# Performance work log

Hardware: AMD Instinct MI355X
Metric: run time of the kernel (lower is better)

## Reference

```python
import jax, jax.numpy as jnp
import numpy as np

N_TEXT = 80000
N_NON = 20000
N = N_TEXT + N_NON
E = 200000
EMB = 256
HID = 256
R = 500
V = 17
MDIM = 64
K = 4
NUM_ROUNDS = 2
NUM_REV_ROUNDS = 2


def setup_inputs():
    key = jax.random.key(0)
    ks = jax.random.split(key, 32)
    f = jnp.float32
    s = 0.05
    inp = {}
    inp["h_id_tensor"] = jax.random.randint(ks[0], (E,), 0, N)
    inp["r_id_tensor"] = jax.random.randint(ks[1], (E,), 0, R)
    inp["t_id_tensor"] = jax.random.randint(ks[2], (E,), 0, N)
    inp["q_emb"] = jax.random.normal(ks[3], (1, EMB), f)
    inp["entity_embs"] = jax.random.normal(ks[4], (N_TEXT, EMB), f)
    inp["num_non_text_entities"] = N_NON
    inp["relation_embs"] = jax.random.normal(ks[5], (R, EMB), f)
    inp["topic_entity_one_hot"] = (jax.random.uniform(ks[6], (N, 2)) < 0.01).astype(f)
    inp["node_motif_token_ids"] = jax.random.randint(ks[7], (N, K), 0, V)
    inp["node_motif_token_wts"] = jax.random.uniform(ks[8], (N, K), f)
    inp["triple_motif_token_ids"] = jax.random.randint(ks[9], (E, K), 0, V)
    inp["triple_motif_token_wts"] = jax.random.uniform(ks[10], (E, K), f)
    inp["non_text_emb"] = jax.random.normal(ks[11], (EMB,), f) * s
    me = jax.random.normal(ks[12], (V, MDIM), f) * s
    inp["motif_emb"] = me.at[0].set(0.0)  # padding_idx=0
    inp["gnn_self_w"] = jax.random.normal(ks[13], (MDIM, MDIM), f) * s
    inp["gnn_self_b"] = jnp.zeros((MDIM,), f)
    inp["gnn_msg_w"] = jax.random.normal(ks[14], (MDIM, MDIM), f) * s
    inp["gnn_msg_b"] = jnp.zeros((MDIM,), f)
    pos_dim = 2 + 2 * (NUM_ROUNDS + NUM_REV_ROUNDS)  # 10
    inp["nh_w"] = jax.random.normal(ks[15], (2 * EMB + 2 * MDIM, HID), f) * s
    inp["nh_b"] = jnp.zeros((HID,), f)
    inp["pos_w"] = jax.random.normal(ks[16], (2 * pos_dim, HID), f) * s
    inp["pos_b"] = jnp.zeros((HID,), f)
    inp["st_w"] = jax.random.normal(ks[17], (EMB + MDIM, HID), f) * s
    inp["st_b"] = jnp.zeros((HID,), f)
    inp["gate_w"] = jax.random.normal(ks[18], (EMB, 3), f) * s
    inp["gate_b"] = jnp.zeros((3,), f)
    inp["pred_w1"] = jax.random.normal(ks[19], (EMB + HID, HID), f) * s
    inp["pred_b1"] = jnp.zeros((HID,), f)
    inp["pred_w2"] = jax.random.normal(ks[20], (HID, 1), f) * s
    inp["pred_b2"] = jnp.zeros((1,), f)
    return inp


def _forward(h_id, r_id, t_id, q_emb, entity_embs, num_non_text, relation_embs,
             topic_oh, node_ids, node_wts, trip_ids, trip_wts,
             non_text_emb, motif_emb, gsw, gsb, gmw, gmb,
             nh_w, nh_b, pos_w, pos_b, st_w, st_b, gate_w, gate_b,
             pw1, pb1, pw2, pb2):
    n = entity_embs.shape[0] + num_non_text
    h_e = jnp.concatenate(
        [entity_embs,
         jnp.broadcast_to(non_text_emb[None, :], (num_non_text, entity_embs.shape[1]))],
        axis=0)  # [N, EMB]
    ones = jnp.ones((h_id.shape[0],), h_e.dtype)
    inv_fwd = 1.0 / jnp.clip(jax.ops.segment_sum(ones, t_id, num_segments=n), 1.0)[:, None]
    inv_rev = 1.0 / jnp.clip(jax.ops.segment_sum(ones, h_id, num_segments=n), 1.0)[:, None]

    def mean_agg(x, src, dst, inv):
        # PyG mean aggregation: mean of source features over incoming edges, 0 if none
        return jax.ops.segment_sum(x[src], dst, num_segments=n) * inv

    dde_list = []
    h = topic_oh
    for _ in range(NUM_ROUNDS):
        h = mean_agg(h, h_id, t_id, inv_fwd)
        dde_list.append(h)
    h = topic_oh
    for _ in range(NUM_REV_ROUNDS):
        h = mean_agg(h, t_id, h_id, inv_rev)
        dde_list.append(h)

    # ---- motif co-occurrence adjacency (vectorized form of the K x K loop) ----
    contrib = trip_wts[:, :, None] * trip_wts[:, None, :]                 # [E,K,K]
    valid = (trip_ids[:, :, None] > 0) & (trip_ids[:, None, :] > 0) & (contrib > 0)
    contrib = jnp.where(valid, contrib, 0.0)
    idx = (trip_ids[:, :, None] * V + trip_ids[:, None, :]).reshape(-1)
    adj = jnp.zeros((V * V,), contrib.dtype).at[idx].add(contrib.reshape(-1)).reshape(V, V)
    adj = 0.5 * (adj + adj.T) + jnp.eye(V, dtype=adj.dtype)
    adj = adj.at[0, :].set(0.0).at[:, 0].set(0.0).at[0, 0].set(1.0)
    adj = adj / jnp.clip(adj.sum(axis=1, keepdims=True), 1e-8)

    # ---- semantic GNN over the motif table ----
    ht = motif_emb
    for _ in range(1):  # semantic_gnn_num_layers = 1, dropout 0 (eval)
        msg = adj @ ht
        ht = ht + jax.nn.relu(ht @ gsw + gsb + msg @ gmw + gmb)

    node_motif_emb = (ht[node_ids] * node_wts[:, :, None]).sum(axis=1)    # [N,MDIM]
    triple_motif_emb = (ht[trip_ids] * trip_wts[:, :, None]).sum(axis=1)  # [E,MDIM]

    h_r = relation_embs[r_id]                                             # [E,EMB]
    h_nbr = jax.nn.relu(
        jnp.concatenate([h_e[h_id], h_e[t_id], node_motif_emb[h_id], node_motif_emb[t_id]],
                        axis=1) @ nh_w + nh_b)
    pos_feat = jnp.concatenate([topic_oh] + dde_list, axis=1)             # [N,10]
    h_pos = jax.nn.relu(
        jnp.concatenate([pos_feat[h_id], pos_feat[t_id]], axis=1) @ pos_w + pos_b)
    h_str = jax.nn.relu(jnp.concatenate([h_r, triple_motif_emb], axis=1) @ st_w + st_b)

    gate = jax.nn.softmax((q_emb @ gate_w + gate_b)[0])                   # [3]
    h_fused = gate[0] * h_nbr + gate[1] * h_pos + gate[2] * h_str
    pred_in = jnp.concatenate(
        [jnp.broadcast_to(q_emb, (h_r.shape[0], q_emb.shape[1])), h_fused], axis=1)
    return jax.nn.relu(pred_in @ pw1 + pb1) @ pw2 + pb2                   # [E,1]


def reference(h_id_tensor, r_id_tensor, t_id_tensor, q_emb, entity_embs,
              num_non_text_entities, relation_embs, topic_entity_one_hot,
              node_motif_token_ids, node_motif_token_wts,
              triple_motif_token_ids, triple_motif_token_wts,
              non_text_emb, motif_emb, gnn_self_w, gnn_self_b, gnn_msg_w, gnn_msg_b,
              nh_w, nh_b, pos_w, pos_b, st_w, st_b, gate_w, gate_b,
              pred_w1, pred_b1, pred_w2, pred_b2):
    return _forward(h_id_tensor, r_id_tensor, t_id_tensor, q_emb, entity_embs,
                    num_non_text_entities, relation_embs, topic_entity_one_hot,
                    node_motif_token_ids, node_motif_token_wts,
                    triple_motif_token_ids, triple_motif_token_wts,
                    non_text_emb, motif_emb, gnn_self_w, gnn_self_b, gnn_msg_w, gnn_msg_b,
                    nh_w, nh_b, pos_w, pos_b, st_w, st_b, gate_w, gate_b,
                    pred_w1, pred_b1, pred_w2, pred_b2)
```

## Files before the change

kernel.cpp:

```cpp
#include <hip/hip_runtime.h>
#include <hip/hip_bf16.h>

#define N_TEXT 80000
#define NTOT   100000
#define NE     200000
#define EMB    256
#define HID    256
#define VMOT   17
#define MDIM   64
#define KTOK   4

typedef unsigned short u16;
typedef unsigned int   u32;
typedef short short8 __attribute__((ext_vector_type(8)));
typedef float f32x4 __attribute__((ext_vector_type(4)));

#define O_INVF 0
#define O_INVR (NTOT)
#define O_POS  (2*NTOT)
#define O_ADJ  (12*NTOT)
#define O_HTB  (12*NTOT + 512)
#define O_GATE (12*NTOT + 1088)
#define O_CVEC (12*NTOT + 1104)
#define O_NME  (12*NTOT + 1360)
#define O_WSW  (O_NME + NTOT*32)
#define ZERO_FLOATS (12*NTOT + 512)
#define Z4 (ZERO_FLOATS/4)

#define GA 20480
#define GB 1024
#define GC 10240
#define GD 8192
#define GTOT (GA+GB+GC+GD)

__device__ __forceinline__ u16 f2b(float f) {
  unsigned u = __float_as_uint(f);
  return (u16)((u + 0x7fffu + ((u >> 16) & 1u)) >> 16);
}
__device__ __forceinline__ float b2f(u16 v) {
  return __uint_as_float(((unsigned)v) << 16);
}
__device__ __forceinline__ short8 pack8f(const float* f) {
  union { u32 u[4]; short8 s; } o;
#pragma unroll
  for (int i = 0; i < 4; i++) {
    __hip_bfloat162 b = __float22bfloat162_rn(float2{f[2*i], f[2*i+1]});
    o.u[i] = *reinterpret_cast<u32*>(&b);
  }
  return o.s;
}

__global__ void k_prep(const float* __restrict__ nh_w, const float* __restrict__ pos_w,
                       const float* __restrict__ st_w, const float* __restrict__ pw1,
                       float* __restrict__ ws) {
  int g = blockIdx.x * blockDim.x + threadIdx.x;
  if (g < Z4) { ((float4*)ws)[g] = make_float4(0.f, 0.f, 0.f, 0.f); return; }
  g -= Z4;
  if (g >= GTOT) return;
  int l, phase;
  if (g < GA) { l = g; phase = 0; }
  else if (g < GA + GB) { l = g - GA; phase = 1; }
  else if (g < GA + GB + GC) { l = g - GA - GB; phase = 2; }
  else { l = g - GA - GB - GC; phase = 3; }
  int c = l >> 10, r = l & 1023;
  int w = r >> 8, nt = (r >> 6) & 3, ln = r & 63;
  int col = w*64 + nt*16 + (ln & 15);
  int k0  = c*32 + ((ln >> 4) << 3);
  float f[8];
#pragma unroll
  for (int j = 0; j < 8; j++) {
    int k = k0 + j;
    float v = 0.f;
    if (phase == 0)      v = nh_w[k*256 + col];
    else if (phase == 1) { if (k < 10) v = pos_w[k*256 + col];
                           else if (k >= 16 && k < 26) v = pos_w[(k-6)*256 + col]; }
    else if (phase == 2) v = st_w[k*256 + col];
    else                 v = pw1[(256 + k)*256 + col];
    f[j] = v;
  }
  ((short8*)((u16*)(ws + O_WSW)))[g] = pack8f(f);
}

__global__ void k_deg_dde1_adj(const int* __restrict__ h_id, const int* __restrict__ t_id,
                               const float* __restrict__ topic,
                               const int* __restrict__ tids, const float* __restrict__ twts,
                               float* __restrict__ ws) {
  __shared__ float sadj[4*304];
  for (int i = threadIdx.x; i < 4*304; i += blockDim.x) sadj[i] = 0.f;
  __syncthreads();
  int wbase = (threadIdx.x >> 6) * 304;
  int e = blockIdx.x * blockDim.x + threadIdx.x;
  if (e < NE) {
    int h = h_id[e], t = t_id[e];
    atomicAdd(&ws[O_INVF + t], 1.0f);
    atomicAdd(&ws[O_INVR + h], 1.0f);
    float hx = topic[2*h], hy = topic[2*h + 1];
    float tx = topic[2*t], ty = topic[2*t + 1];
    if (hx != 0.f) atomicAdd(&ws[O_POS + t*10 + 2], hx);
    if (hy != 0.f) atomicAdd(&ws[O_POS + t*10 + 3], hy);
    if (tx != 0.f) atomicAdd(&ws[O_POS + h*10 + 6], tx);
    if (ty != 0.f) atomicAdd(&ws[O_POS + h*10 + 7], ty);
    int id[KTOK]; float w[KTOK];
#pragma unroll
    for (int k = 0; k < KTOK; k++) { id[k] = tids[e*KTOK + k]; w[k] = twts[e*KTOK + k]; }
#pragma unroll
    for (int i = 0; i < KTOK; i++)
#pragma unroll
      for (int j = 0; j < KTOK; j++) {
        float c = w[i] * w[j];
        if (id[i] > 0 && id[j] > 0 && c > 0.f)
          atomicAdd(&sadj[wbase + id[i]*VMOT + id[j]], c);
      }
  }
  __syncthreads();
  for (int i = threadIdx.x; i < VMOT*VMOT; i += blockDim.x) {
    float v = sadj[i] + sadj[304 + i] + sadj[608 + i] + sadj[912 + i];
    if (v != 0.f) atomicAdd(&ws[O_ADJ + i], v);
  }
}

#define NPN_BLOCKS ((NTOT + 255)/256)
__global__ void k_pnm(const float* __restrict__ topic, const float* __restrict__ mo,
                      const float* __restrict__ gsw, const float* __restrict__ gsb,
                      const float* __restrict__ gmw, const float* __restrict__ gmb,
                      const float* __restrict__ q, const float* __restrict__ gate_w,
                      const float* __restrict__ gate_b, const float* __restrict__ pw1,
                      const float* __restrict__ pb1, float* __restrict__ ws) {
  int t = threadIdx.x;
  if (blockIdx.x < NPN_BLOCKS) {
    int n = blockIdx.x * 256 + t;
    if (n >= NTOT) return;
    float invf = 1.0f / fmaxf(ws[O_INVF + n], 1.0f);
    float invr = 1.0f / fmaxf(ws[O_INVR + n], 1.0f);
    ws[O_INVF + n] = invf;
    ws[O_INVR + n] = invr;
    float* p = &ws[O_POS + n*10];
    p[0] = topic[2*n]; p[1] = topic[2*n + 1];
    p[2] *= invf; p[3] *= invf;
    p[6] *= invr; p[7] *= invr;
  } else if (blockIdx.x == NPN_BLOCKS) {
    __shared__ float A[VMOT*VMOT];
    __shared__ float Bm[VMOT*VMOT];
    __shared__ float inv_row[VMOT];
    __shared__ float smo[VMOT*MDIM];
    __shared__ float sm[VMOT*MDIM];
    for (int i = t; i < VMOT*VMOT; i += 256) A[i] = ws[O_ADJ + i];
    for (int i = t; i < VMOT*MDIM; i += 256) smo[i] = mo[i];
    __syncthreads();
    for (int i = t; i < VMOT*VMOT; i += 256) {
      int r = i / VMOT, c = i % VMOT;
      float v = 0.5f * (A[i] + A[c*VMOT + r]) + (r == c ? 1.f : 0.f);
      if (r == 0 || c == 0) v = (r == 0 && c == 0) ? 1.f : 0.f;
      Bm[i] = v;
    }
    __syncthreads();
    if (t < VMOT) {
      float s = 0.f;
      for (int c = 0; c < VMOT; c++) s += Bm[t*VMOT + c];
      inv_row[t] = 1.f / fmaxf(s, 1e-8f);
    }
    __syncthreads();
    for (int i = t; i < VMOT*MDIM; i += 256) {
      int v = i / MDIM, d = i % MDIM;
      float s = 0.f;
      for (int u = 0; u < VMOT; u++) s += Bm[v*VMOT + u] * smo[u*MDIM + d];
      sm[i] = s * inv_row[v];
    }
    __syncthreads();
    for (int i = t; i < VMOT*MDIM; i += 256) {
      int v = i / MDIM, d = i % MDIM;
      float a = gsb[d] + gmb[d];
      for (int m = 0; m < MDIM; m++)
        a += smo[v*MDIM + m] * gsw[m*MDIM + d] + sm[v*MDIM + m] * gmw[m*MDIM + d];
      ((u16*)(ws + O_HTB))[i] = f2b(smo[i] + fmaxf(a, 0.f));
    }
  } else {
    __shared__ float sq[EMB];
    __shared__ float red[3];
    sq[t] = q[t];
    if (t < 3) red[t] = 0.f;
    __syncthreads();
    float s = pb1[t];
    for (int i = 0; i < EMB; i++) s += sq[i] * pw1[i*HID + t];
    ws[O_CVEC + t] = s;
    atomicAdd(&red[0], sq[t] * gate_w[t*3 + 0]);
    atomicAdd(&red[1], sq[t] * gate_w[t*3 + 1]);
    atomicAdd(&red[2], sq[t] * gate_w[t*3 + 2]);
    __syncthreads();
    if (t == 0) {
      float l0 = red[0] + gate_b[0], l1 = red[1] + gate_b[1], l2 = red[2] + gate_b[2];
      float mx = fmaxf(l0, fmaxf(l1, l2));
      float e0 = expf(l0 - mx), e1 = expf(l1 - mx), e2 = expf(l2 - mx);
      float inv = 1.f / (e0 + e1 + e2);
      ws[O_GATE + 0] = e0 * inv; ws[O_GATE + 1] = e1 * inv; ws[O_GATE + 2] = e2 * inv;
    }
  }
}

__global__ void k_dde2(const int* __restrict__ h_id, const int* __restrict__ t_id,
                       float* __restrict__ ws) {
  int e = blockIdx.x * blockDim.x + threadIdx.x;
  if (e >= NE) return;
  int h = h_id[e], t = t_id[e];
  float a = ws[O_POS + h*10 + 2], b = ws[O_POS + h*10 + 3];
  float c = ws[O_POS + t*10 + 6], d = ws[O_POS + t*10 + 7];
  if (a != 0.f) atomicAdd(&ws[O_POS + t*10 + 4], a);
  if (b != 0.f) atomicAdd(&ws[O_POS + t*10 + 5], b);
  if (c != 0.f) atomicAdd(&ws[O_POS + h*10 + 8], c);
  if (d != 0.f) atomicAdd(&ws[O_POS + h*10 + 9], d);
}

__global__ void k_scale_nme(const int* __restrict__ nids, const float* __restrict__ nwts,
                            float* __restrict__ ws) {
  __shared__ u16 sht[VMOT*MDIM];
  for (int i = threadIdx.x; i < (VMOT*MDIM)/2; i += blockDim.x)
    ((u32*)sht)[i] = ((const u32*)(ws + O_HTB))[i];
  __syncthreads();
  int gid = blockIdx.x * blockDim.x + threadIdx.x;
  if (gid < NTOT) {
    float invf = ws[O_INVF + gid], invr = ws[O_INVR + gid];
    float* p = &ws[O_POS + gid*10];
    p[4] *= invf; p[5] *= invf;
    p[8] *= invr; p[9] *= invr;
  }
  if (gid >= NTOT * 8) return;
  int n = gid >> 3, d0 = (gid & 7) * 8;
  int4   iv = ((const int4*)nids)[n];
  float4 wv = ((const float4*)nwts)[n];
  float f[8];
#pragma unroll
  for (int j = 0; j < 8; j++) {
    f[j] = wv.x * b2f(sht[iv.x*MDIM + d0 + j]) + wv.y * b2f(sht[iv.y*MDIM + d0 + j])
         + wv.z * b2f(sht[iv.z*MDIM + d0 + j]) + wv.w * b2f(sht[iv.w*MDIM + d0 + j]);
  }
  ((short8*)((u16*)(ws + O_NME)))[gid] = pack8f(f);
}

__global__ __launch_bounds__(256, 4) void k_edge_mfma(
    const int* __restrict__ h_id, const int* __restrict__ r_id, const int* __restrict__ t_id,
    const float* __restrict__ ent, const float* __restrict__ rel, const float* __restrict__ nte,
    const int* __restrict__ tids, const float* __restrict__ twts,
    const float* __restrict__ nh_b, const float* __restrict__ pos_b,
    const float* __restrict__ st_b, const float* __restrict__ pw2,
    const float* __restrict__ pb2,
    const float* __restrict__ ws, float* __restrict__ out) {
  __shared__ __align__(16) u16 sX[2][2048];
  __shared__ __align__(16) u16 sF[16384];

  const int tid = threadIdx.x;
  const int wv = tid >> 6, ln = tid & 63;
  const int lm = ln & 15, lq = ln >> 4;
  const int cb = wv * 64;
  const int e0 = blockIdx.x * 64;
  const int srow = tid >> 2, sks = tid & 3;
  const int xoff = (srow >> 4)*512 + (sks*16 + (srow & 15))*8;

  const int   hS = h_id[e0 + srow];
  const int   tS = t_id[e0 + srow];
  const int   rS = r_id[e0 + srow];
  const int4   tivS = ((const int4*)tids)[e0 + srow];
  const float4 twvS = ((const float4*)twts)[e0 + srow];

  const float g0 = ws[O_GATE + 0], g1 = ws[O_GATE + 1], g2 = ws[O_GATE + 2];
  const u16* blob = (const u16*)(ws + O_WSW);
  const u16* nmeb = (const u16*)(ws + O_NME);
  const u16* htb  = (const u16*)(ws + O_HTB);

  f32x4 acc[4][4];
#pragma unroll
  for (int mt = 0; mt < 4; mt++)
#pragma unroll
    for (int nt = 0; nt < 4; nt++) acc[mt][nt] = (f32x4){0.f, 0.f, 0.f, 0.f};

#define MFMA_STEP(buf, bc)                                               \
  { short8 a[4], b[4];                                                   \
    _Pragma("unroll")                                                    \
    for (int nt = 0; nt < 4; nt++)                                       \
      b[nt] = *(const short8*)&blob[(bc)*8192 + wv*2048 + nt*512 + ln*8];\
    _Pragma("unroll")                                                    \
    for (int mt = 0; mt < 4; mt++)                                       \
      a[mt] = *(const short8*)&sX[buf][mt*512 + ln*8];                   \
    _Pragma("unroll")                                                    \
    for (int mt = 0; mt < 4; mt++)                                       \
      _Pragma("unroll")                                                  \
      for (int nt = 0; nt < 4; nt++)                                     \
        acc[mt][nt] = __builtin_amdgcn_mfma_f32_16x16x32_bf16(a[mt], b[nt], acc[mt][nt], 0, 0, 0); }


  float4 fa, fb; short8 xs;
  auto loadA = [&](int c) {
    int kk = c*32 + sks*8;
    if (kk < 512) {
      int node = (kk < 256) ? hS : tS;
      int k2 = kk & 255;
      const float* src = (node < N_TEXT) ? &ent[(size_t)node*256 + k2] : &nte[k2];
      fa = *(const float4*)src; fb = *(const float4*)(src + 4);
    } else {
      int node = (kk < 576) ? hS : tS;
      xs = *(const short8*)&nmeb[(size_t)node*64 + ((kk - 512) & 63)];
    }
  };
  auto storeA = [&](int buf, int c) {
    if (c < 16) {
      float f[8] = {fa.x, fa.y, fa.z, fa.w, fb.x, fb.y, fb.z, fb.w};
      *(short8*)&sX[buf][xoff] = pack8f(f);
    } else {
      *(short8*)&sX[buf][xoff] = xs;
    }
  };
  auto loadC = [&](int c) {
    int kk = c*32 + sks*8;
    if (kk < 256) {
      const float* src = &rel[(size_t)rS*256 + kk];
      fa = *(const float4*)src; fb = *(const float4*)(src + 4);
    } else {
      int d0 = kk - 256;
      short8 h0 = *(const short8*)&htb[tivS.x*64 + d0];
      short8 h1 = *(const short8*)&htb[tivS.y*64 + d0];
      short8 h2 = *(const short8*)&htb[tivS.z*64 + d0];
      short8 h3 = *(const short8*)&htb[tivS.w*64 + d0];
      float f[8];
#pragma unroll
      for (int j = 0; j < 8; j++)
        f[j] = twvS.x * b2f((u16)h0[j]) + twvS.y * b2f((u16)h1[j])
             + twvS.z * b2f((u16)h2[j]) + twvS.w * b2f((u16)h3[j]);
      xs = pack8f(f);
    }
  };
  auto storeC = [&](int buf, int c) {
    if (c < 8) {
      float f[8] = {fa.x, fa.y, fa.z, fa.w, fb.x, fb.y, fb.z, fb.w};
      *(short8*)&sX[buf][xoff] = pack8f(f);
    } else {
      *(short8*)&sX[buf][xoff] = xs;
    }
  };

  loadA(0); storeA(0, 0);
  for (int c = 0; c < 20; c++) {
    __syncthreads();
    if (c < 19) loadA(c + 1);
    MFMA_STEP(c & 1, c);
    if (c < 19) {
      storeA((c + 1) & 1, c + 1);
    } else {
      float f[8];
#pragma unroll
      for (int j = 0; j < 8; j++) {
        int kk = sks*8 + j;
        float v = 0.f;
        if (kk < 10) v = ws[O_POS + (size_t)hS*10 + kk];
        else if (kk >= 16 && kk < 26) v = ws[O_POS + (size_t)tS*10 + kk - 16];
        f[j] = v;
      }
      *(short8*)&sX[0][xoff] = pack8f(f);
    }
  }
#pragma unroll
  for (int nt = 0; nt < 4; nt++) {
    int col = cb + nt*16 + lm;
    float bb = nh_b[col];
    int base = (col >> 5)*2048 + ((col >> 3) & 3)*128 + (col & 7);
#pragma unroll
    for (int mt = 0; mt < 4; mt++)
#pragma unroll
      for (int r = 0; r < 4; r++) {
        sF[base + mt*512 + (lq*4 + r)*8] = f2b(g0 * fmaxf(acc[mt][nt][r] + bb, 0.f));
        acc[mt][nt][r] = 0.f;
      }
  }

  __syncthreads();
  MFMA_STEP(0, 20);
  loadC(0);
#pragma unroll
  for (int nt = 0; nt < 4; nt++) {
    int col = cb + nt*16 + lm;
    float bb = pos_b[col];
    int base = (col >> 5)*2048 + ((col >> 3) & 3)*128 + (col & 7);
#pragma unroll
    for (int mt = 0; mt < 4; mt++)
#pragma unroll
      for (int r = 0; r < 4; r++) {
        u16* p = &sF[base + mt*512 + (lq*4 + r)*8];
        *p = f2b(b2f(*p) + g1 * fmaxf(acc[mt][nt][r] + bb, 0.f));
        acc[mt][nt][r] = 0.f;
      }
  }
  storeC(1, 0);

  for (int c = 0; c < 10; c++) {
    __syncthreads();
    if (c < 9) loadC(c + 1);
    MFMA_STEP((c + 1) & 1, 21 + c);
    if (c < 9) storeC(c & 1, c + 1);
  }
#pragma unroll
  for (int nt = 0; nt < 4; nt++) {
    int col = cb + nt*16 + lm;
    float bb = st_b[col];
    int base = (col >> 5)*2048 + ((col >> 3) & 3)*128 + (col & 7);
#pragma unroll
    for (int mt = 0; mt < 4; mt++)
#pragma unroll
      for (int r = 0; r < 4; r++) {
        u16* p = &sF[base + mt*512 + (lq*4 + r)*8];
        *p = f2b(b2f(*p) + g2 * fmaxf(acc[mt][nt][r] + bb, 0.f));
        acc[mt][nt][r] = 0.f;
      }
  }

  __syncthreads();

#pragma unroll 2
  for (int c = 0; c < 8; c++) {
    short8 a[4], b[4];
#pragma unroll
    for (int nt = 0; nt < 4; nt++)
      b[nt] = *(const short8*)&blob[(31 + c)*8192 + wv*2048 + nt*512 + ln*8];
#pragma unroll
    for (int mt = 0; mt < 4; mt++)
      a[mt] = *(const short8*)&sF[c*2048 + mt*512 + ln*8];
#pragma unroll
    for (int mt = 0; mt < 4; mt++)
#pragma unroll
      for (int nt = 0; nt < 4; nt++)
        acc[mt][nt] = __builtin_amdgcn_mfma_f32_16x16x32_bf16(a[mt], b[nt], acc[mt][nt], 0, 0, 0);
  }

  __syncthreads();
  float* sOut = (float*)sF;
  if (tid < 64) sOut[tid] = 0.f;
  __syncthreads();
  {
    float cv[4], p2[4];
#pragma unroll
    for (int nt = 0; nt < 4; nt++) {
      int col = cb + nt*16 + lm;
      cv[nt] = ws[O_CVEC + col];
      p2[nt] = pw2[col];
    }
#pragma unroll
    for (int mt = 0; mt < 4; mt++)
#pragma unroll
      for (int r = 0; r < 4; r++) {
        float s = 0.f;
#pragma unroll
        for (int nt = 0; nt < 4; nt++)
          s += fmaxf(acc[mt][nt][r] + cv[nt], 0.f) * p2[nt];
#pragma unroll
        for (int off = 1; off < 16; off <<= 1)
          s += __shfl_xor(s, off, 64);
        if (lm == 0) atomicAdd(&sOut[mt*16 + lq*4 + r], s);
      }
  }
  __syncthreads();
  if (tid < 64) out[e0 + tid] = sOut[tid] + pb2[0];
#undef MFMA_STEP
}

extern "C" void kernel_launch(void* const* d_in, const int* in_sizes, int n_in,
                              void* d_out, int out_size, void* d_ws, size_t ws_size,
                              hipStream_t stream) {
  (void)in_sizes; (void)n_in; (void)out_size; (void)ws_size;
  const int*   h_id   = (const int*)  d_in[0];
  const int*   r_id   = (const int*)  d_in[1];
  const int*   t_id   = (const int*)  d_in[2];
  const float* q      = (const float*)d_in[3];
  const float* ent    = (const float*)d_in[4];
  const float* rel    = (const float*)d_in[6];
  const float* topic  = (const float*)d_in[7];
  const int*   nids   = (const int*)  d_in[8];
  const float* nwts   = (const float*)d_in[9];
  const int*   tids   = (const int*)  d_in[10];
  const float* twts   = (const float*)d_in[11];
  const float* nte    = (const float*)d_in[12];
  const float* mo     = (const float*)d_in[13];
  const float* gsw    = (const float*)d_in[14];
  const float* gsb    = (const float*)d_in[15];
  const float* gmw    = (const float*)d_in[16];
  const float* gmb    = (const float*)d_in[17];
  const float* nh_w   = (const float*)d_in[18];
  const float* nh_b   = (const float*)d_in[19];
  const float* pos_w  = (const float*)d_in[20];
  const float* pos_b  = (const float*)d_in[21];
  const float* st_w   = (const float*)d_in[22];
  const float* st_b   = (const float*)d_in[23];
  const float* gate_w = (const float*)d_in[24];
  const float* gate_b = (const float*)d_in[25];
  const float* pw1    = (const float*)d_in[26];
  const float* pb1    = (const float*)d_in[27];
  const float* pw2    = (const float*)d_in[28];
  const float* pb2    = (const float*)d_in[29];
  float* ws  = (float*)d_ws;
  float* out = (float*)d_out;

  k_prep<<<(Z4 + GTOT + 255)/256, 256, 0, stream>>>(nh_w, pos_w, st_w, pw1, ws);
  k_deg_dde1_adj<<<(NE + 255)/256, 256, 0, stream>>>(h_id, t_id, topic, tids, twts, ws);
  k_pnm<<<NPN_BLOCKS + 2, 256, 0, stream>>>(topic, mo, gsw, gsb, gmw, gmb,
                                            q, gate_w, gate_b, pw1, pb1, ws);
  k_dde2<<<(NE + 255)/256, 256, 0, stream>>>(h_id, t_id, ws);
  k_scale_nme<<<(NTOT*8 + 255)/256, 256, 0, stream>>>(nids, nwts, ws);
  k_edge_mfma<<<NE/64, 256, 0, stream>>>(h_id, r_id, t_id, ent, rel, nte, tids, twts,
                                         nh_b, pos_b, st_b, pw2, pb2, ws, out);
}
```

Baseline: 495.0 us.

## Unify edge GEMM stages into one pipelined loop with register-prefetched weights

The three separate staged loops in the edge MFMA kernel (node-half, positional, structural) become one fully unrolled 31-step loop. It prefetches weight fragments into double-buffered registers and gathers activations two steps ahead, with the per-stage epilogues folded in at fixed steps. The final prediction GEMM also reuses the register-prefetched weights. Separately, workspace zeroing moves to hipMemsetAsync and the weight-packing and degree/adjacency kernels merge into one launch. Occupancy is lowered from 4 to 3 blocks per SM to make room for the extra registers, which may reduce latency hiding.

```diff
diff --git a/kernel.cpp b/kernel.cpp
--- a/kernel.cpp
+++ b/kernel.cpp
@@ -25,13 +25,14 @@
 #define O_NME  (12*NTOT + 1360)
 #define O_WSW  (O_NME + NTOT*32)
 #define ZERO_FLOATS (12*NTOT + 512)
-#define Z4 (ZERO_FLOATS/4)
 
 #define GA 20480
 #define GB 1024
 #define GC 10240
 #define GD 8192
 #define GTOT (GA+GB+GC+GD)
+#define PREPB ((GTOT + 255)/256)
+#define EDGEB ((NE + 255)/256)
 
 __device__ __forceinline__ u16 f2b(float f) {
   unsigned u = __float_as_uint(f);
@@ -50,72 +51,70 @@
   return o.s;
 }
 
-__global__ void k_prep(const float* __restrict__ nh_w, const float* __restrict__ pos_w,
+__global__ void k_init(const float* __restrict__ nh_w, const float* __restrict__ pos_w,
                        const float* __restrict__ st_w, const float* __restrict__ pw1,
+                       const int* __restrict__ h_id, const int* __restrict__ t_id,
+                       const float* __restrict__ topic,
+                       const int* __restrict__ tids, const float* __restrict__ twts,
                        float* __restrict__ ws) {
-  int g = blockIdx.x * blockDim.x + threadIdx.x;
-  if (g < Z4) { ((float4*)ws)[g] = make_float4(0.f, 0.f, 0.f, 0.f); return; }
-  g -= Z4;
-  if (g >= GTOT) return;
-  int l, phase;
-  if (g < GA) { l = g; phase = 0; }
-  else if (g < GA + GB) { l = g - GA; phase = 1; }
-  else if (g < GA + GB + GC) { l = g - GA - GB; phase = 2; }
-  else { l = g - GA - GB - GC; phase = 3; }
-  int c = l >> 10, r = l & 1023;
-  int w = r >> 8, nt = (r >> 6) & 3, ln = r & 63;
-  int col = w*64 + nt*16 + (ln & 15);
-  int k0  = c*32 + ((ln >> 4) << 3);
-  float f[8];
-#pragma unroll
-  for (int j = 0; j < 8; j++) {
-    int k = k0 + j;
-    float v = 0.f;
-    if (phase == 0)      v = nh_w[k*256 + col];
-    else if (phase == 1) { if (k < 10) v = pos_w[k*256 + col];
-                           else if (k >= 16 && k < 26) v = pos_w[(k-6)*256 + col]; }
-    else if (phase == 2) v = st_w[k*256 + col];
-    else                 v = pw1[(256 + k)*256 + col];
-    f[j] = v;
-  }
-  ((short8*)((u16*)(ws + O_WSW)))[g] = pack8f(f);
-}
-
-__global__ void k_deg_dde1_adj(const int* __restrict__ h_id, const int* __restrict__ t_id,
-                               const float* __restrict__ topic,
-                               const int* __restrict__ tids, const float* __restrict__ twts,
-                               float* __restrict__ ws) {
   __shared__ float sadj[4*304];
-  for (int i = threadIdx.x; i < 4*304; i += blockDim.x) sadj[i] = 0.f;
-  __syncthreads();
-  int wbase = (threadIdx.x >> 6) * 304;
-  int e = blockIdx.x * blockDim.x + threadIdx.x;
-  if (e < NE) {
-    int h = h_id[e], t = t_id[e];
-    atomicAdd(&ws[O_INVF + t], 1.0f);
-    atomicAdd(&ws[O_INVR + h], 1.0f);
-    float hx = topic[2*h], hy = topic[2*h + 1];
-    float tx = topic[2*t], ty = topic[2*t + 1];
-    if (hx != 0.f) atomicAdd(&ws[O_POS + t*10 + 2], hx);
-    if (hy != 0.f) atomicAdd(&ws[O_POS + t*10 + 3], hy);
-    if (tx != 0.f) atomicAdd(&ws[O_POS + h*10 + 6], tx);
-    if (ty != 0.f) atomicAdd(&ws[O_POS + h*10 + 7], ty);
-    int id[KTOK]; float w[KTOK];
-#pragma unroll
-    for (int k = 0; k < KTOK; k++) { id[k] = tids[e*KTOK + k]; w[k] = twts[e*KTOK + k]; }
-#pragma unroll
-    for (int i = 0; i < KTOK; i++)
-#pragma unroll
-      for (int j = 0; j < KTOK; j++) {
-        float c = w[i] * w[j];
-        if (id[i] > 0 && id[j] > 0 && c > 0.f)
-          atomicAdd(&sadj[wbase + id[i]*VMOT + id[j]], c);
-      }
-  }
-  __syncthreads();
-  for (int i = threadIdx.x; i < VMOT*VMOT; i += blockDim.x) {
-    float v = sadj[i] + sadj[304 + i] + sadj[608 + i] + sadj[912 + i];
-    if (v != 0.f) atomicAdd(&ws[O_ADJ + i], v);
+  if (blockIdx.x < PREPB) {
+    int g = blockIdx.x * 256 + threadIdx.x;
+    if (g >= GTOT) return;
+    int l, phase;
+    if (g < GA) { l = g; phase = 0; }
+    else if (g < GA + GB) { l = g - GA; phase = 1; }
+    else if (g < GA + GB + GC) { l = g - GA - GB; phase = 2; }
+    else { l = g - GA - GB - GC; phase = 3; }
+    int c = l >> 10, r = l & 1023;
+    int w = r >> 8, nt = (r >> 6) & 3, ln = r & 63;
+    int col = w*64 + nt*16 + (ln & 15);
+    int k0  = c*32 + ((ln >> 4) << 3);
+    float f[8];
+#pragma unroll
+    for (int j = 0; j < 8; j++) {
+      int k = k0 + j;
+      float v = 0.f;
+      if (phase == 0)      v = nh_w[k*256 + col];
+      else if (phase == 1) { if (k < 10) v = pos_w[k*256 + col];
+                             else if (k >= 16 && k < 26) v = pos_w[(k-6)*256 + col]; }
+      else if (phase == 2) v = st_w[k*256 + col];
+      else                 v = pw1[(256 + k)*256 + col];
+      f[j] = v;
+    }
+    ((short8*)((u16*)(ws + O_WSW)))[g] = pack8f(f);
+  } else {
+    for (int i = threadIdx.x; i < 4*304; i += blockDim.x) sadj[i] = 0.f;
+    __syncthreads();
+    int wbase = (threadIdx.x >> 6) * 304;
+    int e = (blockIdx.x - PREPB) * 256 + threadIdx.x;
+    if (e < NE) {
+      int h = h_id[e], t = t_id[e];
+      atomicAdd(&ws[O_INVF + t], 1.0f);
+      atomicAdd(&ws[O_INVR + h], 1.0f);
+      float hx = topic[2*h], hy = topic[2*h + 1];
+      float tx = topic[2*t], ty = topic[2*t + 1];
+      if (hx != 0.f) atomicAdd(&ws[O_POS + t*10 + 2], hx);
+      if (hy != 0.f) atomicAdd(&ws[O_POS + t*10 + 3], hy);
+      if (tx != 0.f) atomicAdd(&ws[O_POS + h*10 + 6], tx);
+      if (ty != 0.f) atomicAdd(&ws[O_POS + h*10 + 7], ty);
+      int id[KTOK]; float w[KTOK];
+#pragma unroll
+      for (int k = 0; k < KTOK; k++) { id[k] = tids[e*KTOK + k]; w[k] = twts[e*KTOK + k]; }
+#pragma unroll
+      for (int i = 0; i < KTOK; i++)
+#pragma unroll
+        for (int j = 0; j < KTOK; j++) {
+          float c = w[i] * w[j];
+          if (id[i] > 0 && id[j] > 0 && c > 0.f)
+            atomicAdd(&sadj[wbase + id[i]*VMOT + id[j]], c);
+        }
+    }
+    __syncthreads();
+    for (int i = threadIdx.x; i < VMOT*VMOT; i += blockDim.x) {
+      float v = sadj[i] + sadj[304 + i] + sadj[608 + i] + sadj[912 + i];
+      if (v != 0.f) atomicAdd(&ws[O_ADJ + i], v);
+    }
   }
 }
 
@@ -236,7 +235,7 @@
   ((short8*)((u16*)(ws + O_NME)))[gid] = pack8f(f);
 }
 
-__global__ __launch_bounds__(256, 4) void k_edge_mfma(
+__global__ __launch_bounds__(256, 3) void k_edge_mfma(
     const int* __restrict__ h_id, const int* __restrict__ r_id, const int* __restrict__ t_id,
     const float* __restrict__ ent, const float* __restrict__ rel, const float* __restrict__ nte,
     const int* __restrict__ tids, const float* __restrict__ twts,
@@ -272,78 +271,22 @@
 #pragma unroll
     for (int nt = 0; nt < 4; nt++) acc[mt][nt] = (f32x4){0.f, 0.f, 0.f, 0.f};
 
-#define MFMA_STEP(buf, bc)                                               \
-  { short8 a[4], b[4];                                                   \
-    _Pragma("unroll")                                                    \
-    for (int nt = 0; nt < 4; nt++)                                       \
-      b[nt] = *(const short8*)&blob[(bc)*8192 + wv*2048 + nt*512 + ln*8];\
-    _Pragma("unroll")                                                    \
-    for (int mt = 0; mt < 4; mt++)                                       \
-      a[mt] = *(const short8*)&sX[buf][mt*512 + ln*8];                   \
-    _Pragma("unroll")                                                    \
-    for (int mt = 0; mt < 4; mt++)                                       \
-      _Pragma("unroll")                                                  \
-      for (int nt = 0; nt < 4; nt++)                                     \
-        acc[mt][nt] = __builtin_amdgcn_mfma_f32_16x16x32_bf16(a[mt], b[nt], acc[mt][nt], 0, 0, 0); }
-
-
-  float4 fa, fb; short8 xs;
-  auto loadA = [&](int c) {
-    int kk = c*32 + sks*8;
-    if (kk < 512) {
+  float4 gfa[2], gfb[2]; short8 gxs[2];
+  short8 breg[2][4];
+
+  auto gatherX = [&](int k) {
+    int p = k & 1;
+    if (k < 16) {
+      int kk = k*32 + sks*8;
       int node = (kk < 256) ? hS : tS;
       int k2 = kk & 255;
       const float* src = (node < N_TEXT) ? &ent[(size_t)node*256 + k2] : &nte[k2];
-      fa = *(const float4*)src; fb = *(const float4*)(src + 4);
-    } else {
+      gfa[p] = *(const float4*)src; gfb[p] = *(const float4*)(src + 4);
+    } else if (k < 20) {
+      int kk = k*32 + sks*8;
       int node = (kk < 576) ? hS : tS;
-      xs = *(const short8*)&nmeb[(size_t)node*64 + ((kk - 512) & 63)];
-    }
-  };
-  auto storeA = [&](int buf, int c) {
-    if (c < 16) {
-      float f[8] = {fa.x, fa.y, fa.z, fa.w, fb.x, fb.y, fb.z, fb.w};
-      *(short8*)&sX[buf][xoff] = pack8f(f);
-    } else {
-      *(short8*)&sX[buf][xoff] = xs;
-    }
-  };
-  auto loadC = [&](int c) {
-    int kk = c*32 + sks*8;
-    if (kk < 256) {
-      const float* src = &rel[(size_t)rS*256 + kk];
-      fa = *(const float4*)src; fb = *(const float4*)(src + 4);
-    } else {
-      int d0 = kk - 256;
-      short8 h0 = *(const short8*)&htb[tivS.x*64 + d0];
-      short8 h1 = *(const short8*)&htb[tivS.y*64 + d0];
-      short8 h2 = *(const short8*)&htb[tivS.z*64 + d0];
-      short8 h3 = *(const short8*)&htb[tivS.w*64 + d0];
-      float f[8];
-#pragma unroll
-      for (int j = 0; j < 8; j++)
-        f[j] = twvS.x * b2f((u16)h0[j]) + twvS.y * b2f((u16)h1[j])
-             + twvS.z * b2f((u16)h2[j]) + twvS.w * b2f((u16)h3[j]);
-      xs = pack8f(f);
-    }
-  };
-  auto storeC = [&](int buf, int c) {
-    if (c < 8) {
-      float f[8] = {fa.x, fa.y, fa.z, fa.w, fb.x, fb.y, fb.z, fb.w};
-      *(short8*)&sX[buf][xoff] = pack8f(f);
-    } else {
-      *(short8*)&sX[buf][xoff] = xs;
-    }
-  };
-
-  loadA(0); storeA(0, 0);
-  for (int c = 0; c < 20; c++) {
-    __syncthreads();
-    if (c < 19) loadA(c + 1);
-    MFMA_STEP(c & 1, c);
-    if (c < 19) {
-      storeA((c + 1) & 1, c + 1);
-    } else {
+      gxs[p] = *(const short8*)&nmeb[(size_t)node*64 + ((kk - 512) & 63)];
+    } else if (k == 20) {
       float f[8];
 #pragma unroll
       for (int j = 0; j < 8; j++) {
@@ -353,71 +296,104 @@
         else if (kk >= 16 && kk < 26) v = ws[O_POS + (size_t)tS*10 + kk - 16];
         f[j] = v;
       }
-      *(short8*)&sX[0][xoff] = pack8f(f);
-    }
-  }
-#pragma unroll
-  for (int nt = 0; nt < 4; nt++) {
-    int col = cb + nt*16 + lm;
-    float bb = nh_b[col];
-    int base = (col >> 5)*2048 + ((col >> 3) & 3)*128 + (col & 7);
-#pragma unroll
-    for (int mt = 0; mt < 4; mt++)
-#pragma unroll
-      for (int r = 0; r < 4; r++) {
-        sF[base + mt*512 + (lq*4 + r)*8] = f2b(g0 * fmaxf(acc[mt][nt][r] + bb, 0.f));
-        acc[mt][nt][r] = 0.f;
-      }
+      gxs[p] = pack8f(f);
+    } else if (k < 29) {
+      int kk = (k - 21)*32 + sks*8;
+      const float* src = &rel[(size_t)rS*256 + kk];
+      gfa[p] = *(const float4*)src; gfb[p] = *(const float4*)(src + 4);
+    } else {
+      int d0 = (k - 21)*32 + sks*8 - 256;
+      short8 h0 = *(const short8*)&htb[tivS.x*64 + d0];
+      short8 h1 = *(const short8*)&htb[tivS.y*64 + d0];
+      short8 h2 = *(const short8*)&htb[tivS.z*64 + d0];
+      short8 h3 = *(const short8*)&htb[tivS.w*64 + d0];
+      float f[8];
+#pragma unroll
+      for (int j = 0; j < 8; j++)
+        f[j] = twvS.x * b2f((u16)h0[j]) + twvS.y * b2f((u16)h1[j])
+             + twvS.z * b2f((u16)h2[j]) + twvS.w * b2f((u16)h3[j]);
+      gxs[p] = pack8f(f);
+    }
+  };
+  auto storeX = [&](int k) {
+    int p = k & 1;
+    if (k < 16 || (k >= 21 && k < 29)) {
+      float f[8] = {gfa[p].x, gfa[p].y, gfa[p].z, gfa[p].w,
+                    gfb[p].x, gfb[p].y, gfb[p].z, gfb[p].w};
+      *(short8*)&sX[p][xoff] = pack8f(f);
+    } else {
+      *(short8*)&sX[p][xoff] = gxs[p];
+    }
+  };
+  auto bload = [&](int bc, int p) {
+#pragma unroll
+    for (int nt = 0; nt < 4; nt++)
+      breg[p][nt] = *(const short8*)&blob[(size_t)bc*8192 + wv*2048 + nt*512 + ln*8];
+  };
+  auto epi_store = [&](const float* __restrict__ bias, float g) {
+#pragma unroll
+    for (int nt = 0; nt < 4; nt++) {
+      int col = cb + nt*16 + lm;
+      float bb = bias[col];
+      int base = (col >> 5)*2048 + ((col >> 3) & 3)*128 + (col & 7);
+#pragma unroll
+      for (int mt = 0; mt < 4; mt++)
+#pragma unroll
+        for (int r = 0; r < 4; r++) {
+          sF[base + mt*512 + (lq*4 + r)*8] = f2b(g * fmaxf(acc[mt][nt][r] + bb, 0.f));
+          acc[mt][nt][r] = 0.f;
+        }
+    }
+  };
+  auto epi_rmw = [&](const float* __restrict__ bias, float g) {
+#pragma unroll
+    for (int nt = 0; nt < 4; nt++) {
+      int col = cb + nt*16 + lm;
+      float bb = bias[col];
+      int base = (col >> 5)*2048 + ((col >> 3) & 3)*128 + (col & 7);
+#pragma unroll
+      for (int mt = 0; mt < 4; mt++)
+#pragma unroll
+        for (int r = 0; r < 4; r++) {
+          u16* p = &sF[base + mt*512 + (lq*4 + r)*8];
+          *p = f2b(b2f(*p) + g * fmaxf(acc[mt][nt][r] + bb, 0.f));
+          acc[mt][nt][r] = 0.f;
+        }
+    }
+  };
+
+  gatherX(0); gatherX(1);
+  bload(0, 0);
+  storeX(0);
+
+#pragma unroll
+  for (int c = 0; c < 31; c++) {
+    __syncthreads();
+    {
+      short8 a[4];
+#pragma unroll
+      for (int mt = 0; mt < 4; mt++)
+        a[mt] = *(const short8*)&sX[c & 1][mt*512 + ln*8];
+#pragma unroll
+      for (int mt = 0; mt < 4; mt++)
+#pragma unroll
+        for (int nt = 0; nt < 4; nt++)
+          acc[mt][nt] = __builtin_amdgcn_mfma_f32_16x16x32_bf16(
+              a[mt], breg[c & 1][nt], acc[mt][nt], 0, 0, 0);
+    }
+    if (c < 30) storeX(c + 1);
+    bload(c + 1, (c + 1) & 1);
+    if (c < 29) gatherX(c + 2);
+    if (c == 19) epi_store(nh_b, g0);
+    if (c == 20) epi_rmw(pos_b, g1);
+    if (c == 30) epi_rmw(st_b, g2);
   }
 
   __syncthreads();
-  MFMA_STEP(0, 20);
-  loadC(0);
-#pragma unroll
-  for (int nt = 0; nt < 4; nt++) {
-    int col = cb + nt*16 + lm;
-    float bb = pos_b[col];
-    int base = (col >> 5)*2048 + ((col >> 3) & 3)*128 + (col & 7);
-#pragma unroll
-    for (int mt = 0; mt < 4; mt++)
-#pragma unroll
-      for (int r = 0; r < 4; r++) {
-        u16* p = &sF[base + mt*512 + (lq*4 + r)*8];
-        *p = f2b(b2f(*p) + g1 * fmaxf(acc[mt][nt][r] + bb, 0.f));
-        acc[mt][nt][r] = 0.f;
-      }
-  }
-  storeC(1, 0);
-
-  for (int c = 0; c < 10; c++) {
-    __syncthreads();
-    if (c < 9) loadC(c + 1);
-    MFMA_STEP((c + 1) & 1, 21 + c);
-    if (c < 9) storeC(c & 1, c + 1);
-  }
-#pragma unroll
-  for (int nt = 0; nt < 4; nt++) {
-    int col = cb + nt*16 + lm;
-    float bb = st_b[col];
-    int base = (col >> 5)*2048 + ((col >> 3) & 3)*128 + (col & 7);
-#pragma unroll
-    for (int mt = 0; mt < 4; mt++)
-#pragma unroll
-      for (int r = 0; r < 4; r++) {
-        u16* p = &sF[base + mt*512 + (lq*4 + r)*8];
-        *p = f2b(b2f(*p) + g2 * fmaxf(acc[mt][nt][r] + bb, 0.f));
-        acc[mt][nt][r] = 0.f;
-      }
-  }
-
-  __syncthreads();
-
-#pragma unroll 2
+
+#pragma unroll
   for (int c = 0; c < 8; c++) {
-    short8 a[4], b[4];
-#pragma unroll
-    for (int nt = 0; nt < 4; nt++)
-      b[nt] = *(const short8*)&blob[(31 + c)*8192 + wv*2048 + nt*512 + ln*8];
+    short8 a[4];
 #pragma unroll
     for (int mt = 0; mt < 4; mt++)
       a[mt] = *(const short8*)&sF[c*2048 + mt*512 + ln*8];
@@ -425,7 +401,9 @@
     for (int mt = 0; mt < 4; mt++)
 #pragma unroll
       for (int nt = 0; nt < 4; nt++)
-        acc[mt][nt] = __builtin_amdgcn_mfma_f32_16x16x32_bf16(a[mt], b[nt], acc[mt][nt], 0, 0, 0);
+        acc[mt][nt] = __builtin_amdgcn_mfma_f32_16x16x32_bf16(
+            a[mt], breg[(31 + c) & 1][nt], acc[mt][nt], 0, 0, 0);
+    if (c < 7) bload(32 + c, (32 + c) & 1);
   }
 
   __syncthreads();
@@ -456,7 +434,6 @@
   }
   __syncthreads();
   if (tid < 64) out[e0 + tid] = sOut[tid] + pb2[0];
-#undef MFMA_STEP
 }
 
 extern "C" void kernel_launch(void* const* d_in, const int* in_sizes, int n_in,
@@ -495,8 +472,9 @@
   float* ws  = (float*)d_ws;
   float* out = (float*)d_out;
 
-  k_prep<<<(Z4 + GTOT + 255)/256, 256, 0, stream>>>(nh_w, pos_w, st_w, pw1, ws);
-  k_deg_dde1_adj<<<(NE + 255)/256, 256, 0, stream>>>(h_id, t_id, topic, tids, twts, ws);
+  hipMemsetAsync(ws, 0, (size_t)ZERO_FLOATS * sizeof(float), stream);
+  k_init<<<PREPB + EDGEB, 256, 0, stream>>>(nh_w, pos_w, st_w, pw1,
+                                            h_id, t_id, topic, tids, twts, ws);
   k_pnm<<<NPN_BLOCKS + 2, 256, 0, stream>>>(topic, mo, gsw, gsb, gmw, gmb,
                                             q, gate_w, gate_b, pw1, pb1, ws);
   k_dde2<<<(NE + 255)/256, 256, 0, stream>>>(h_id, t_id, ws);
```

Measured after the change: 439.3 us. -11.2%, faster.
